# Performance work log

Hardware: AMD Instinct MI355X
Metric: run time of the kernel (lower is better)

Reference implementation:

```python
import jax, jax.numpy as jnp
import numpy as np

HIDDEN = 2048
NUM_HEADS = 16
HEAD_DIM = 128
WINDOW_SIZE = 512
NUM_GLOBAL = 16
SCALING = HEAD_DIM ** -0.5


def setup_inputs() -> dict:
    key = jax.random.key(0)
    ks = jax.random.split(key, 5)
    std = HIDDEN ** -0.5
    hidden_states = jax.random.normal(ks[0], (1, 4096, HIDDEN), dtype=jnp.float32)
    # Linear weights stored as (in, out) so y = x @ W
    Wq = jax.random.normal(ks[1], (HIDDEN, NUM_HEADS * HEAD_DIM), dtype=jnp.float32) * std
    Wk = jax.random.normal(ks[2], (HIDDEN, NUM_HEADS * HEAD_DIM), dtype=jnp.float32) * std
    Wv = jax.random.normal(ks[3], (HIDDEN, NUM_HEADS * HEAD_DIM), dtype=jnp.float32) * std
    Wo = jax.random.normal(ks[4], (NUM_HEADS * HEAD_DIM, HIDDEN), dtype=jnp.float32) * std
    return {"hidden_states": hidden_states, "Wq": Wq, "Wk": Wk, "Wv": Wv, "Wo": Wo}


def _sliding_mask(q_len: int, kv_len: int) -> jnp.ndarray:
    q_pos = jnp.arange(q_len)[:, None]
    kv_pos = jnp.arange(kv_len)[None, :]
    half_window = WINDOW_SIZE // 2
    local = jnp.abs(q_pos - kv_pos) < half_window
    glob = (q_pos < NUM_GLOBAL) | (kv_pos < NUM_GLOBAL)
    mask = local | glob
    return jnp.where(mask, 0.0, -jnp.inf).astype(jnp.float32)


def reference(hidden_states, Wq, Wk, Wv, Wo):
    bsz, q_len, _ = hidden_states.shape
    q = (hidden_states @ Wq).reshape(bsz, q_len, NUM_HEADS, HEAD_DIM).transpose(0, 2, 1, 3)
    k = (hidden_states @ Wk).reshape(bsz, q_len, NUM_HEADS, HEAD_DIM).transpose(0, 2, 1, 3)
    v = (hidden_states @ Wv).reshape(bsz, q_len, NUM_HEADS, HEAD_DIM).transpose(0, 2, 1, 3)
    mask = _sliding_mask(q_len, q_len)[None, None]  # [1,1,S,S]
    scores = jnp.einsum("bhqd,bhkd->bhqk", q, k) * SCALING + mask
    attn = jax.nn.softmax(scores.astype(jnp.float32), axis=-1).astype(q.dtype)
    out = jnp.einsum("bhqk,bhkd->bhqd", attn, v)
    out = out.transpose(0, 2, 1, 3).reshape(bsz, q_len, NUM_HEADS * HEAD_DIM)
    return out @ Wo
```

## Files before the change

kernel.cpp:

```cpp
#include <hip/hip_runtime.h>
#include <stdint.h>

#define SEQ    4096
#define HID    2048
#define NQKV   6144
#define NH     16
#define HD     128
#define SCALE  0.08838834764831845f
#define GQC    32

typedef unsigned short u16;
typedef __attribute__((ext_vector_type(8))) short bf16x8;
typedef __attribute__((ext_vector_type(4))) float f32x4;

__device__ __forceinline__ u16 f2bf(float f) {
  union { float f; unsigned u; } v; v.f = f;
  unsigned r = v.u + 0x7FFFu + ((v.u >> 16) & 1u);
  return (u16)(r >> 16);
}

__device__ __forceinline__ float bf2f(u16 b) {
  union { unsigned u; float f; } c; c.u = ((unsigned)b) << 16; return c.f;
}

__device__ __forceinline__ void async16(const u16* g, u16* l) {
  __builtin_amdgcn_global_load_lds(
      (const __attribute__((address_space(1))) unsigned int*)g,
      (__attribute__((address_space(3))) unsigned int*)l, 16, 0, 0);
}

__global__ __launch_bounds__(256) void cvt_f32_bf16(const float* __restrict__ in,
                                                    u16* __restrict__ out, int n4) {
  int i = blockIdx.x * 256 + threadIdx.x;
  if (i >= n4) return;
  float4 v = ((const float4*)in)[i];
  ushort4 o;
  o.x = f2bf(v.x); o.y = f2bf(v.y); o.z = f2bf(v.z); o.w = f2bf(v.w);
  ((ushort4*)out)[i] = o;
}

__global__ __launch_bounds__(256) void transpose_w4(const float* __restrict__ W0,
                                                    const float* __restrict__ W1,
                                                    const float* __restrict__ W2,
                                                    const float* __restrict__ W3,
                                                    u16* __restrict__ Wcat,
                                                    u16* __restrict__ Wot) {
  __shared__ __align__(16) u16 Ts[64 * 72];
  const int n0 = blockIdx.x * 64;
  const int k0 = blockIdx.y * 64;
  const int z = blockIdx.z;
  const float* W = (z == 0) ? W0 : (z == 1) ? W1 : (z == 2) ? W2 : W3;
  u16* Wt = (z < 3) ? (Wcat + (size_t)z * 2048 * 2048) : Wot;
  const int t = threadIdx.x;
#pragma unroll
  for (int p = 0; p < 4; ++p) {
    int f = (t + p * 256) * 4;
    int r = f >> 6, c = f & 63;
    float4 v = *(const float4*)&W[(size_t)(k0 + r) * 2048 + n0 + c];
    ushort4 o; o.x = f2bf(v.x); o.y = f2bf(v.y); o.z = f2bf(v.z); o.w = f2bf(v.w);
    *(ushort4*)&Ts[r * 72 + c] = o;
  }
  __syncthreads();
#pragma unroll
  for (int p = 0; p < 4; ++p) {
    int g = (t + p * 256) * 4;
    int r = g >> 6, c = g & 63;
    ushort4 o;
    o.x = Ts[(c + 0) * 72 + r];
    o.y = Ts[(c + 1) * 72 + r];
    o.z = Ts[(c + 2) * 72 + r];
    o.w = Ts[(c + 3) * 72 + r];
    *(ushort4*)&Wt[(size_t)(n0 + r) * 2048 + k0 + c] = o;
  }
}

__global__ __launch_bounds__(256) void transpose_v(const u16* __restrict__ qkv,
                                                   u16* __restrict__ vt) {
  __shared__ __align__(16) u16 Ts[64 * 72];
  const int s0 = blockIdx.x * 64;
  const int d0 = blockIdx.y * 64;
  const int h = blockIdx.z;
  const int t = threadIdx.x;
#pragma unroll
  for (int p = 0; p < 2; ++p) {
    int f = (t + p * 256) * 8;
    int r = f >> 6, c = f & 63;
    uint4 v = *(const uint4*)&qkv[(size_t)(s0 + r) * NQKV + 4096 + h * HD + d0 + c];
    *(uint4*)&Ts[r * 72 + c] = v;
  }
  __syncthreads();
#pragma unroll
  for (int p = 0; p < 2; ++p) {
    int g = (t + p * 256) * 8;
    int r = g >> 6, c = g & 63;
    u16 tmp[8];
#pragma unroll
    for (int j = 0; j < 8; ++j) tmp[j] = Ts[(c + j) * 72 + r];
    *(uint4*)&vt[(size_t)h * (HD * SEQ) + (size_t)(d0 + r) * SEQ + s0 + c] = *(uint4*)tmp;
  }
}

template <typename OutT>
__global__ __launch_bounds__(256) void gemm_bt(const u16* __restrict__ A,
                                               const u16* __restrict__ B,
                                               OutT* __restrict__ C,
                                               int K, int ldc) {
  __shared__ __align__(16) u16 As[128 * 32];
  __shared__ __align__(16) u16 Bs[128 * 32];
  const int m0 = blockIdx.y * 128;
  const int n0 = blockIdx.x * 128;
  const int tid = threadIdx.x;
  const int wid = tid >> 6;
  const int lane = tid & 63;
  const int wm = wid & 1, wn = wid >> 1;
  const int l15 = lane & 15, g4 = lane >> 4;

  const int srow = wid * 32 + (lane >> 2);
  const int scol = (lane & 3) * 8;

  f32x4 acc[4][4] = {};

  const u16* pa0 = &A[(size_t)(m0 + srow) * K + scol];
  const u16* pa1 = &A[(size_t)(m0 + srow + 16) * K + scol];
  const u16* pb0 = &B[(size_t)(n0 + srow) * K + scol];
  const u16* pb1 = &B[(size_t)(n0 + srow + 16) * K + scol];
  u16* la0 = &As[(wid * 32) * 32];
  u16* la1 = &As[(wid * 32 + 16) * 32];
  u16* lb0 = &Bs[(wid * 32) * 32];
  u16* lb1 = &Bs[(wid * 32 + 16) * 32];

  for (int kt = 0; kt < K; kt += 32) {
    __syncthreads();
    async16(pa0 + kt, la0);
    async16(pa1 + kt, la1);
    async16(pb0 + kt, lb0);
    async16(pb1 + kt, lb1);
    __syncthreads();
    bf16x8 af[4], bfr[4];
#pragma unroll
    for (int i = 0; i < 4; ++i)
      af[i] = *(const bf16x8*)&As[(wm * 64 + i * 16 + l15) * 32 + g4 * 8];
#pragma unroll
    for (int i = 0; i < 4; ++i)
      bfr[i] = *(const bf16x8*)&Bs[(wn * 64 + i * 16 + l15) * 32 + g4 * 8];
#pragma unroll
    for (int mi = 0; mi < 4; ++mi)
#pragma unroll
      for (int ni = 0; ni < 4; ++ni)
        acc[mi][ni] = __builtin_amdgcn_mfma_f32_16x16x32_bf16(af[mi], bfr[ni], acc[mi][ni], 0, 0, 0);
  }
#pragma unroll
  for (int mi = 0; mi < 4; ++mi)
#pragma unroll
    for (int ni = 0; ni < 4; ++ni) {
      const int n = n0 + wn * 64 + ni * 16 + l15;
#pragma unroll
      for (int r = 0; r < 4; ++r) {
        const int m = m0 + wm * 64 + mi * 16 + g4 * 4 + r;
        float v = acc[mi][ni][r];
        if constexpr (sizeof(OutT) == 2) {
          C[(size_t)m * ldc + n] = (OutT)f2bf(v);
        } else {
          C[(size_t)m * ldc + n] = v;
        }
      }
    }
}

__global__ __launch_bounds__(256, 3) void attn_kernel(const u16* __restrict__ qkv,
                                                      const u16* __restrict__ vt,
                                                      u16* __restrict__ out) {
  __shared__ __align__(16) u16 Ks[64 * 128];
  __shared__ __align__(16) u16 VTs[128 * 64];
  __shared__ __align__(16) u16 Ps[64 * 64];
  const int q0 = blockIdx.x * 64;
  const int h = blockIdx.y;
  const int tid = threadIdx.x;
  const int w = tid >> 6;
  const int lane = tid & 63;
  const int l15 = lane & 15, g4 = lane >> 4;
  const int l7 = l15 & 7;

  bf16x8 qf[4];
  {
    const u16* qrow = &qkv[(size_t)(q0 + w * 16 + l15) * NQKV + h * HD + g4 * 8];
#pragma unroll
    for (int kk = 0; kk < 4; ++kk) qf[kk] = *(const bf16x8*)&qrow[kk * 32];
  }

  float m_run = -1e30f, l_run = 0.f;
  f32x4 o[8] = {};

  int lo = q0 - 255;
  int lo_blk = (lo < 0) ? 0 : (lo >> 6);
  int hi_blk = (q0 + 318) >> 6;
  if (hi_blk > 63) hi_blk = 63;
  const int extra = (lo_blk > 0) ? 1 : 0;
  const int nsteps = hi_blk - lo_blk + 1 + extra;

  for (int step = 0; step < nsteps; ++step) {
    const int kb = (extra && step == 0) ? 0 : (lo_blk + step - extra);
    const int kv0 = kb * 64;
    __syncthreads();
#pragma unroll
    for (int p = 0; p < 4; ++p) {
      int id = p * 256 + tid;
      int r = id >> 4, c8 = id & 15;
      uint4 v = *(const uint4*)&qkv[(size_t)(kv0 + r) * NQKV + 2048 + h * HD + c8 * 8];
      *(uint4*)&Ks[r * 128 + ((c8 ^ (r & 15)) * 8)] = v;
    }
#pragma unroll
    for (int p = 0; p < 4; ++p) {
      int id = p * 256 + tid;
      int r = id >> 3, c8 = id & 7;
      uint4 v = *(const uint4*)&vt[(size_t)h * (HD * SEQ) + (size_t)r * SEQ + kv0 + c8 * 8];
      *(uint4*)&VTs[r * 64 + ((c8 ^ (r & 7)) * 8)] = v;
    }
    __syncthreads();

    f32x4 st[4] = {};
#pragma unroll
    for (int kk = 0; kk < 4; ++kk) {
#pragma unroll
      for (int t4 = 0; t4 < 4; ++t4) {
        bf16x8 ak = *(const bf16x8*)&Ks[(t4 * 16 + l15) * 128 + (((kk * 4 + g4) ^ l15) * 8)];
        st[t4] = __builtin_amdgcn_mfma_f32_16x16x32_bf16(ak, qf[kk], st[t4], 0, 0, 0);
      }
    }

    const int q = q0 + w * 16 + l15;
    float pv[4][4];
    float cmax = -1e30f;
#pragma unroll
    for (int t4 = 0; t4 < 4; ++t4)
#pragma unroll
      for (int r = 0; r < 4; ++r) {
        int kv = kv0 + t4 * 16 + g4 * 4 + r;
        int dq = q - kv; if (dq < 0) dq = -dq;
        bool ok = (dq < 256) || (kv < 16);
        float s = ok ? st[t4][r] * SCALE : -1e30f;
        pv[t4][r] = s;
        cmax = fmaxf(cmax, s);
      }
    cmax = fmaxf(cmax, __shfl_xor(cmax, 16, 64));
    cmax = fmaxf(cmax, __shfl_xor(cmax, 32, 64));
    float mnew = fmaxf(m_run, cmax);
    float csum = 0.f;
#pragma unroll
    for (int t4 = 0; t4 < 4; ++t4)
#pragma unroll
      for (int r = 0; r < 4; ++r) {
        float p = __expf(pv[t4][r] - mnew);
        pv[t4][r] = p;
        csum += p;
      }
    csum += __shfl_xor(csum, 16, 64);
    csum += __shfl_xor(csum, 32, 64);
    float alpha = __expf(m_run - mnew);
    m_run = mnew;
    l_run = l_run * alpha + csum;

#pragma unroll
    for (int t4 = 0; t4 < 4; ++t4) {
      u16 pk[4];
#pragma unroll
      for (int r = 0; r < 4; ++r) pk[r] = f2bf(pv[t4][r]);
      int c8 = t4 * 2 + (g4 >> 1);
      *(uint2*)&Ps[(w * 16 + l15) * 64 + ((c8 ^ l7) * 8) + (g4 & 1) * 4] = *(uint2*)pk;
    }

    float al[4];
#pragma unroll
    for (int r = 0; r < 4; ++r) al[r] = __shfl(alpha, g4 * 4 + r, 64);
#pragma unroll
    for (int nt = 0; nt < 8; ++nt)
#pragma unroll
      for (int r = 0; r < 4; ++r) o[nt][r] *= al[r];

#pragma unroll
    for (int ks = 0; ks < 2; ++ks) {
      bf16x8 ap = *(const bf16x8*)&Ps[(w * 16 + l15) * 64 + (((ks * 4 + g4) ^ l7) * 8)];
#pragma unroll
      for (int nt = 0; nt < 8; ++nt) {
        bf16x8 bv = *(const bf16x8*)&VTs[(nt * 16 + l15) * 64 + (((ks * 4 + g4) ^ l7) * 8)];
        o[nt] = __builtin_amdgcn_mfma_f32_16x16x32_bf16(ap, bv, o[nt], 0, 0, 0);
      }
    }
  }

  float lr[4];
#pragma unroll
  for (int r = 0; r < 4; ++r) lr[r] = 1.f / __shfl(l_run, g4 * 4 + r, 64);
#pragma unroll
  for (int nt = 0; nt < 8; ++nt)
#pragma unroll
    for (int r = 0; r < 4; ++r) {
      const int m = q0 + w * 16 + g4 * 4 + r;
      if (m < 16) continue;
      const int n = h * HD + nt * 16 + l15;
      out[(size_t)m * HID + n] = f2bf(o[nt][r] * lr[r]);
    }
}

__global__ __launch_bounds__(256) void attn_global(const u16* __restrict__ qkv,
                                                   float* __restrict__ Opart,
                                                   float* __restrict__ MLpart) {
  __shared__ __align__(16) u16 Ks[64 * 136];
  __shared__ __align__(16) u16 Vs[64 * 136];
  const int chunk = blockIdx.x, h = blockIdx.y;
  const int t = threadIdx.x;
  const int q = t >> 4, dg = t & 15;

  float qr[8];
  {
    bf16x8 v = *(const bf16x8*)&qkv[(size_t)q * NQKV + h * HD + dg * 8];
#pragma unroll
    for (int j = 0; j < 8; ++j) qr[j] = bf2f((u16)v[j]);
  }
  float m_run = -1e30f, l_run = 0.f, o[8] = {};
  const int kvbase = chunk * (SEQ / GQC);

  for (int st = 0; st < (SEQ / GQC) / 64; ++st) {
    const int kv0 = kvbase + st * 64;
    __syncthreads();
#pragma unroll
    for (int p = 0; p < 4; ++p) {
      int f = (t + p * 256) * 8;
      int r = f >> 7, c = f & 127;
      *(uint4*)&Ks[r * 136 + c] = *(const uint4*)&qkv[(size_t)(kv0 + r) * NQKV + 2048 + h * HD + c];
      *(uint4*)&Vs[r * 136 + c] = *(const uint4*)&qkv[(size_t)(kv0 + r) * NQKV + 4096 + h * HD + c];
    }
    __syncthreads();
    for (int kv = 0; kv < 64; ++kv) {
      bf16x8 kr = *(const bf16x8*)&Ks[kv * 136 + dg * 8];
      float s = 0.f;
#pragma unroll
      for (int j = 0; j < 8; ++j) s += qr[j] * bf2f((u16)kr[j]);
      s += __shfl_xor(s, 1, 64); s += __shfl_xor(s, 2, 64);
      s += __shfl_xor(s, 4, 64); s += __shfl_xor(s, 8, 64);
      s *= SCALE;
      float mnew = fmaxf(m_run, s);
      float alpha = __expf(m_run - mnew);
      float p = __expf(s - mnew);
      m_run = mnew;
      l_run = l_run * alpha + p;
      bf16x8 vr = *(const bf16x8*)&Vs[kv * 136 + dg * 8];
#pragma unroll
      for (int j = 0; j < 8; ++j) o[j] = o[j] * alpha + p * bf2f((u16)vr[j]);
    }
  }
  float* op = &Opart[(((size_t)h * GQC + chunk) * 16 + q) * HD + dg * 8];
#pragma unroll
  for (int j = 0; j < 8; ++j) op[j] = o[j];
  if (dg == 0) {
    float* ml = &MLpart[(((size_t)h * GQC + chunk) * 16 + q) * 2];
    ml[0] = m_run; ml[1] = l_run;
  }
}

__global__ __launch_bounds__(256) void attn_gred(const float* __restrict__ Opart,
                                                 const float* __restrict__ MLpart,
                                                 u16* __restrict__ out) {
  const int h = blockIdx.x;
  const int t = threadIdx.x;
  const int q = t >> 4, dg = t & 15;
  float M = -1e30f;
  for (int c = 0; c < GQC; ++c)
    M = fmaxf(M, MLpart[(((size_t)h * GQC + c) * 16 + q) * 2]);
  float L = 0.f, o[8] = {};
  for (int c = 0; c < GQC; ++c) {
    const float* ml = &MLpart[(((size_t)h * GQC + c) * 16 + q) * 2];
    float e = __expf(ml[0] - M);
    L += e * ml[1];
    const float* op = &Opart[(((size_t)h * GQC + c) * 16 + q) * HD + dg * 8];
#pragma unroll
    for (int j = 0; j < 8; ++j) o[j] += e * op[j];
  }
  float inv = 1.f / L;
  u16 tmp[8];
#pragma unroll
  for (int j = 0; j < 8; ++j) tmp[j] = f2bf(o[j] * inv);
  *(uint4*)&out[(size_t)q * HID + h * HD + dg * 8] = *(uint4*)tmp;
}

extern "C" void kernel_launch(void* const* d_in, const int* in_sizes, int n_in,
                              void* d_out, int out_size, void* d_ws, size_t ws_size,
                              hipStream_t stream) {
  const float* X  = (const float*)d_in[0];
  const float* Wq = (const float*)d_in[1];
  const float* Wk = (const float*)d_in[2];
  const float* Wv = (const float*)d_in[3];
  const float* Wo = (const float*)d_in[4];
  float* out = (float*)d_out;

  char* ws = (char*)d_ws;
  u16* Xbf    = (u16*)(ws);
  u16* Wcat   = (u16*)(ws + (size_t)(16 << 20));
  u16* VT     = (u16*)(ws);
  u16* AttnO  = (u16*)(ws + (size_t)(16 << 20));
  float* Opart  = (float*)(ws + (size_t)(32 << 20));
  float* MLpart = (float*)(ws + (size_t)(36 << 20));
  u16* QKV    = (u16*)(ws + (size_t)(40 << 20));
  u16* Wot    = (u16*)(ws + (size_t)(88 << 20));

  cvt_f32_bf16<<<dim3(8192), dim3(256), 0, stream>>>(X, Xbf, (SEQ * HID) / 4);
  transpose_w4<<<dim3(32, 32, 4), 256, 0, stream>>>(Wq, Wk, Wv, Wo, Wcat, Wot);
  gemm_bt<u16><<<dim3(48, 32), 256, 0, stream>>>(Xbf, Wcat, QKV, HID, NQKV);
  attn_global<<<dim3(GQC, NH), 256, 0, stream>>>(QKV, Opart, MLpart);
  transpose_v<<<dim3(64, 2, 16), 256, 0, stream>>>(QKV, VT);
  attn_kernel<<<dim3(64, 16), 256, 0, stream>>>(QKV, VT, AttnO);
  attn_gred<<<dim3(NH), 256, 0, stream>>>(Opart, MLpart, AttnO);
  gemm_bt<float><<<dim3(16, 32), 256, 0, stream>>>(AttnO, Wot, out, HID, HID);
}
```

Baseline: 433.2 us.

## Switch GEMM to 32x32 MFMA and write V transposed from QKV epilogue

The GEMM inner loop now uses 32x32x16 bf16 MFMA tiles with 2x2 accumulators in place of 16x16x32 tiles with 4x4 accumulators. The QKV GEMM epilogue writes the V columns straight into a per-head transposed buffer, so the separate transpose_v kernel and the V part of the QKV buffer go away. The global-attention kernel now reads V from the transposed buffer and scatters it back into row layout in shared memory. The intent is to save a kernel launch and a round trip of V through memory. In exchange, the epilogue stores are narrower and strided, and the LDS scatter in attn_global is uncoalesced.

After: 430.6 us. About the same (-0.6%).

```diff
diff --git a/kernel.cpp b/kernel.cpp
--- a/kernel.cpp
+++ b/kernel.cpp
@@ -4,6 +4,7 @@
 #define SEQ    4096
 #define HID    2048
 #define NQKV   6144
+#define QKW    4096
 #define NH     16
 #define HD     128
 #define SCALE  0.08838834764831845f
@@ -12,6 +13,7 @@
 typedef unsigned short u16;
 typedef __attribute__((ext_vector_type(8))) short bf16x8;
 typedef __attribute__((ext_vector_type(4))) float f32x4;
+typedef __attribute__((ext_vector_type(16))) float f32x16;
 
 __device__ __forceinline__ u16 f2bf(float f) {
   union { float f; unsigned u; } v; v.f = f;
@@ -74,36 +76,11 @@
   }
 }
 
-__global__ __launch_bounds__(256) void transpose_v(const u16* __restrict__ qkv,
-                                                   u16* __restrict__ vt) {
-  __shared__ __align__(16) u16 Ts[64 * 72];
-  const int s0 = blockIdx.x * 64;
-  const int d0 = blockIdx.y * 64;
-  const int h = blockIdx.z;
-  const int t = threadIdx.x;
-#pragma unroll
-  for (int p = 0; p < 2; ++p) {
-    int f = (t + p * 256) * 8;
-    int r = f >> 6, c = f & 63;
-    uint4 v = *(const uint4*)&qkv[(size_t)(s0 + r) * NQKV + 4096 + h * HD + d0 + c];
-    *(uint4*)&Ts[r * 72 + c] = v;
-  }
-  __syncthreads();
-#pragma unroll
-  for (int p = 0; p < 2; ++p) {
-    int g = (t + p * 256) * 8;
-    int r = g >> 6, c = g & 63;
-    u16 tmp[8];
-#pragma unroll
-    for (int j = 0; j < 8; ++j) tmp[j] = Ts[(c + j) * 72 + r];
-    *(uint4*)&vt[(size_t)h * (HD * SEQ) + (size_t)(d0 + r) * SEQ + s0 + c] = *(uint4*)tmp;
-  }
-}
-
-template <typename OutT>
+template <typename OutT, bool WVT>
 __global__ __launch_bounds__(256) void gemm_bt(const u16* __restrict__ A,
                                                const u16* __restrict__ B,
                                                OutT* __restrict__ C,
+                                               u16* __restrict__ VTout,
                                                int K, int ldc) {
   __shared__ __align__(16) u16 As[128 * 32];
   __shared__ __align__(16) u16 Bs[128 * 32];
@@ -113,12 +90,12 @@
   const int wid = tid >> 6;
   const int lane = tid & 63;
   const int wm = wid & 1, wn = wid >> 1;
-  const int l15 = lane & 15, g4 = lane >> 4;
+  const int l31 = lane & 31, g2 = lane >> 5;
 
   const int srow = wid * 32 + (lane >> 2);
   const int scol = (lane & 3) * 8;
 
-  f32x4 acc[4][4] = {};
+  f32x16 acc[2][2] = {};
 
   const u16* pa0 = &A[(size_t)(m0 + srow) * K + scol];
   const u16* pa1 = &A[(size_t)(m0 + srow + 16) * K + scol];
@@ -136,38 +113,65 @@
     async16(pb0 + kt, lb0);
     async16(pb1 + kt, lb1);
     __syncthreads();
-    bf16x8 af[4], bfr[4];
-#pragma unroll
-    for (int i = 0; i < 4; ++i)
-      af[i] = *(const bf16x8*)&As[(wm * 64 + i * 16 + l15) * 32 + g4 * 8];
-#pragma unroll
-    for (int i = 0; i < 4; ++i)
-      bfr[i] = *(const bf16x8*)&Bs[(wn * 64 + i * 16 + l15) * 32 + g4 * 8];
-#pragma unroll
-    for (int mi = 0; mi < 4; ++mi)
-#pragma unroll
-      for (int ni = 0; ni < 4; ++ni)
-        acc[mi][ni] = __builtin_amdgcn_mfma_f32_16x16x32_bf16(af[mi], bfr[ni], acc[mi][ni], 0, 0, 0);
-  }
-#pragma unroll
-  for (int mi = 0; mi < 4; ++mi)
-#pragma unroll
-    for (int ni = 0; ni < 4; ++ni) {
-      const int n = n0 + wn * 64 + ni * 16 + l15;
-#pragma unroll
-      for (int r = 0; r < 4; ++r) {
-        const int m = m0 + wm * 64 + mi * 16 + g4 * 4 + r;
-        float v = acc[mi][ni][r];
-        if constexpr (sizeof(OutT) == 2) {
-          C[(size_t)m * ldc + n] = (OutT)f2bf(v);
-        } else {
-          C[(size_t)m * ldc + n] = v;
+    bf16x8 af[2][2], bfr[2][2];
+#pragma unroll
+    for (int ks = 0; ks < 2; ++ks)
+#pragma unroll
+      for (int i = 0; i < 2; ++i) {
+        af[ks][i]  = *(const bf16x8*)&As[(wm * 64 + i * 32 + l31) * 32 + ks * 16 + g2 * 8];
+        bfr[ks][i] = *(const bf16x8*)&Bs[(wn * 64 + i * 32 + l31) * 32 + ks * 16 + g2 * 8];
+      }
+#pragma unroll
+    for (int ks = 0; ks < 2; ++ks)
+#pragma unroll
+      for (int mi = 0; mi < 2; ++mi)
+#pragma unroll
+        for (int ni = 0; ni < 2; ++ni)
+          acc[mi][ni] = __builtin_amdgcn_mfma_f32_32x32x16_bf16(af[ks][mi], bfr[ks][ni],
+                                                                acc[mi][ni], 0, 0, 0);
+  }
+
+  if (WVT && n0 >= QKW) {
+#pragma unroll
+    for (int mi = 0; mi < 2; ++mi)
+#pragma unroll
+      for (int ni = 0; ni < 2; ++ni) {
+        const int nv = n0 - QKW + wn * 64 + ni * 32 + l31;
+        const int hh = nv >> 7, dd = nv & 127;
+        u16* base = &VTout[((size_t)hh * HD + dd) * SEQ];
+#pragma unroll
+        for (int rg = 0; rg < 4; ++rg) {
+          const int mb = m0 + wm * 64 + mi * 32 + rg * 8 + g2 * 4;
+          u16 pk[4];
+#pragma unroll
+          for (int r = 0; r < 4; ++r) pk[r] = f2bf(acc[mi][ni][rg * 4 + r]);
+          *(uint2*)&base[mb] = *(uint2*)pk;
         }
       }
-    }
-}
-
-__global__ __launch_bounds__(256, 3) void attn_kernel(const u16* __restrict__ qkv,
+  } else {
+#pragma unroll
+    for (int mi = 0; mi < 2; ++mi)
+#pragma unroll
+      for (int ni = 0; ni < 2; ++ni) {
+        const int n = n0 + wn * 64 + ni * 32 + l31;
+#pragma unroll
+        for (int rg = 0; rg < 4; ++rg) {
+          const int mb = m0 + wm * 64 + mi * 32 + rg * 8 + g2 * 4;
+#pragma unroll
+          for (int r = 0; r < 4; ++r) {
+            float v = acc[mi][ni][rg * 4 + r];
+            if constexpr (sizeof(OutT) == 2) {
+              C[(size_t)(mb + r) * ldc + n] = (OutT)f2bf(v);
+            } else {
+              C[(size_t)(mb + r) * ldc + n] = v;
+            }
+          }
+        }
+      }
+  }
+}
+
+__global__ __launch_bounds__(256, 3) void attn_kernel(const u16* __restrict__ qk,
                                                       const u16* __restrict__ vt,
                                                       u16* __restrict__ out) {
   __shared__ __align__(16) u16 Ks[64 * 128];
@@ -183,7 +187,7 @@
 
   bf16x8 qf[4];
   {
-    const u16* qrow = &qkv[(size_t)(q0 + w * 16 + l15) * NQKV + h * HD + g4 * 8];
+    const u16* qrow = &qk[(size_t)(q0 + w * 16 + l15) * QKW + h * HD + g4 * 8];
 #pragma unroll
     for (int kk = 0; kk < 4; ++kk) qf[kk] = *(const bf16x8*)&qrow[kk * 32];
   }
@@ -206,7 +210,7 @@
     for (int p = 0; p < 4; ++p) {
       int id = p * 256 + tid;
       int r = id >> 4, c8 = id & 15;
-      uint4 v = *(const uint4*)&qkv[(size_t)(kv0 + r) * NQKV + 2048 + h * HD + c8 * 8];
+      uint4 v = *(const uint4*)&qk[(size_t)(kv0 + r) * QKW + 2048 + h * HD + c8 * 8];
       *(uint4*)&Ks[r * 128 + ((c8 ^ (r & 15)) * 8)] = v;
     }
 #pragma unroll
@@ -302,7 +306,8 @@
     }
 }
 
-__global__ __launch_bounds__(256) void attn_global(const u16* __restrict__ qkv,
+__global__ __launch_bounds__(256) void attn_global(const u16* __restrict__ qk,
+                                                   const u16* __restrict__ vt,
                                                    float* __restrict__ Opart,
                                                    float* __restrict__ MLpart) {
   __shared__ __align__(16) u16 Ks[64 * 136];
@@ -313,7 +318,7 @@
 
   float qr[8];
   {
-    bf16x8 v = *(const bf16x8*)&qkv[(size_t)q * NQKV + h * HD + dg * 8];
+    bf16x8 v = *(const bf16x8*)&qk[(size_t)q * QKW + h * HD + dg * 8];
 #pragma unroll
     for (int j = 0; j < 8; ++j) qr[j] = bf2f((u16)v[j]);
   }
@@ -327,8 +332,16 @@
     for (int p = 0; p < 4; ++p) {
       int f = (t + p * 256) * 8;
       int r = f >> 7, c = f & 127;
-      *(uint4*)&Ks[r * 136 + c] = *(const uint4*)&qkv[(size_t)(kv0 + r) * NQKV + 2048 + h * HD + c];
-      *(uint4*)&Vs[r * 136 + c] = *(const uint4*)&qkv[(size_t)(kv0 + r) * NQKV + 4096 + h * HD + c];
+      *(uint4*)&Ks[r * 136 + c] = *(const uint4*)&qk[(size_t)(kv0 + r) * QKW + 2048 + h * HD + c];
+    }
+#pragma unroll
+    for (int p = 0; p < 4; ++p) {
+      int id = p * 256 + t;
+      int d = id >> 3, c8 = id & 7;
+      uint4 v = *(const uint4*)&vt[(size_t)h * (HD * SEQ) + (size_t)d * SEQ + kv0 + c8 * 8];
+      const u16* pv16 = (const u16*)&v;
+#pragma unroll
+      for (int j = 0; j < 8; ++j) Vs[(c8 * 8 + j) * 136 + d] = pv16[j];
     }
     __syncthreads();
     for (int kv = 0; kv < 64; ++kv) {
@@ -396,19 +409,18 @@
   char* ws = (char*)d_ws;
   u16* Xbf    = (u16*)(ws);
   u16* Wcat   = (u16*)(ws + (size_t)(16 << 20));
-  u16* VT     = (u16*)(ws);
   u16* AttnO  = (u16*)(ws + (size_t)(16 << 20));
   float* Opart  = (float*)(ws + (size_t)(32 << 20));
   float* MLpart = (float*)(ws + (size_t)(36 << 20));
-  u16* QKV    = (u16*)(ws + (size_t)(40 << 20));
+  u16* QK     = (u16*)(ws + (size_t)(40 << 20));
+  u16* VT     = (u16*)(ws + (size_t)(72 << 20));
   u16* Wot    = (u16*)(ws + (size_t)(88 << 20));
 
   cvt_f32_bf16<<<dim3(8192), dim3(256), 0, stream>>>(X, Xbf, (SEQ * HID) / 4);
   transpose_w4<<<dim3(32, 32, 4), 256, 0, stream>>>(Wq, Wk, Wv, Wo, Wcat, Wot);
-  gemm_bt<u16><<<dim3(48, 32), 256, 0, stream>>>(Xbf, Wcat, QKV, HID, NQKV);
-  attn_global<<<dim3(GQC, NH), 256, 0, stream>>>(QKV, Opart, MLpart);
-  transpose_v<<<dim3(64, 2, 16), 256, 0, stream>>>(QKV, VT);
-  attn_kernel<<<dim3(64, 16), 256, 0, stream>>>(QKV, VT, AttnO);
+  gemm_bt<u16, true><<<dim3(48, 32), 256, 0, stream>>>(Xbf, Wcat, QK, VT, HID, QKW);
+  attn_global<<<dim3(GQC, NH), 256, 0, stream>>>(QK, VT, Opart, MLpart);
+  attn_kernel<<<dim3(64, 16), 256, 0, stream>>>(QK, VT, AttnO);
   attn_gred<<<dim3(NH), 256, 0, stream>>>(Opart, MLpart, AttnO);
-  gemm_bt<float><<<dim3(16, 32), 256, 0, stream>>>(AttnO, Wot, out, HID, HID);
-}
+  gemm_bt<float, false><<<dim3(16, 32), 256, 0, stream>>>(AttnO, Wot, out, nullptr, HID, HID);
+}
```
